# Kernel tuning notes

Measured on AMD Instinct MI355X. Metric: run time of the kernel, lower is better.

Reference implementation:

```python
import jax, jax.numpy as jnp
import numpy as np

EPS = 1e-5
TOP_N = 8
NUM_POINTS = 100
OUT_LO, OUT_HI = 0.0, 1.0


def setup_inputs() -> dict:
    key = jax.random.key(0)
    ks = jax.random.split(key, 7)
    B, D, M, R, MO = 2048, 8, 7, 32768, 9
    x = jax.random.normal(ks[0], (B, D), dtype=jnp.float32)
    # antecedent MF index per (rule, input); -1 means input unused in that rule
    antecedents = jax.random.randint(ks[1], (R, D), 0, M + 1) - 1  # values in [-1, M)
    consequents = jax.random.randint(ks[2], (R,), 0, MO)
    in_centers = jax.random.normal(ks[3], (D, M), dtype=jnp.float32)
    in_widths = 0.2 + 0.3 * jax.random.uniform(ks[4], (D, M), dtype=jnp.float32)
    out_centers = jax.random.uniform(ks[5], (MO,), dtype=jnp.float32)
    out_widths = 0.05 + 0.2 * jax.random.uniform(ks[6], (MO,), dtype=jnp.float32)
    return {"x": x, "antecedents": antecedents, "consequents": consequents,
            "in_centers": in_centers, "in_widths": in_widths,
            "out_centers": out_centers, "out_widths": out_widths}


def reference(x, antecedents, consequents, in_centers, in_widths, out_centers, out_widths):
    B, D = x.shape
    R = antecedents.shape[0]
    M = in_centers.shape[1]

    # Fuzzification: Gaussian input MFs, clamped like the torch module. mu: [B, D, M]
    z = (x[:, :, None] - in_centers[None, :, :]) / in_widths[None, :, :]
    mu = jnp.clip(jnp.exp(-0.5 * z * z), EPS, 1.0)

    # Rule firing strengths: product over inputs of selected memberships ([B, R]).
    # Small fixed loop over D (8) keeps peak memory at one [B, R] temp per step.
    firing = jnp.ones((B, R), dtype=x.dtype)
    for i in range(D):
        idx = antecedents[:, i]                      # [R], -1 => unused
        safe = jnp.clip(idx, 0, M - 1)
        vals = mu[:, i, safe]                        # [B, R]
        firing = firing * jnp.where(idx[None, :] == -1, jnp.ones((), x.dtype), vals)

    top_vals, top_idx = jax.lax.top_k(firing, TOP_N)  # [B, TOP_N]

    # Output universe and output MF table: [MO, P]
    universe = jnp.linspace(OUT_LO, OUT_HI, NUM_POINTS, dtype=x.dtype)
    zo = (universe[None, :] - out_centers[:, None]) / out_widths[:, None]
    out_mu = jnp.exp(-0.5 * zo * zo)

    # Mamdani implication (product) + aggregation (sum) + centroid defuzzification
    cons_top = consequents[top_idx]                   # [B, TOP_N]
    implications = top_vals[:, :, None] * out_mu[cons_top]  # [B, TOP_N, P]
    aggregated = implications.sum(axis=1)             # [B, P]
    numerator = (universe[None, :] * aggregated).sum(axis=1)
    denominator = aggregated.sum(axis=1) + EPS
    return numerator / denominator
```

## Files before the change

### kernel.cpp

```cpp
#include <hip/hip_runtime.h>
#include <math.h>

#define DD 8
#define MM 7
#define MOO 9
#define NPTS 100
#define EPSF 1e-5f

#define THREADS 1024
#define ITERS 8
#define ROWS 8
#define CAP 256
#define WLCAP 8192
#define THR_SLACK 0.9879f

__device__ __forceinline__ float bl(unsigned u) { return __uint_as_float(u << 16); }
__device__ __forceinline__ float bh(unsigned u) { return __uint_as_float(u & 0xFFFF0000u); }
__device__ __forceinline__ unsigned pkb(float a, float b) {
    return (__float_as_uint(b) & 0xFFFF0000u) | (__float_as_uint(a) >> 16);
}

__global__ __launch_bounds__(256) void pack_kernel(const int* __restrict__ ant,
                                                   unsigned* __restrict__ g_off,
                                                   int R) {
    int r = blockIdx.x * 256 + threadIdx.x;
    if (r < R) {
        const int4* a = reinterpret_cast<const int4*>(ant) + (size_t)r * 2;
        int4 lo = a[0], hi = a[1];
        int v[8] = {lo.x, lo.y, lo.z, lo.w, hi.x, hi.y, hi.z, hi.w};
        unsigned code = 0u;
        #pragma unroll
        for (int i = 0; i < 8; ++i) {
            int c = v[i];
            c = (c < 0) ? 7 : (c > MM - 1 ? MM - 1 : c);
            code |= (unsigned)c << (3 * i);
        }
        g_off[r] = ((code & 4095u) << 3) | ((((code >> 12) << 3) + 32768u) << 16);
    }
}

__global__ __launch_bounds__(THREADS, 4) void anfis_scan8(
    const float* __restrict__ x,
    const unsigned* __restrict__ stream_off,
    const float* __restrict__ in_centers,
    const float* __restrict__ in_widths,
    float* __restrict__ g_thr,
    unsigned long long* __restrict__ g_bitmap)
{
    __shared__ uint4 quads[8192];
    __shared__ float mu[ROWS][64];
    __shared__ float pairs[ROWS][256];
    __shared__ uint4 smaxpk[THREADS];
    __shared__ float sT[ROWS];

    const int tid = threadIdx.x;
    const int b0  = blockIdx.x * ROWS;

    if (tid < 512) {
        int row = tid >> 6, d = (tid >> 3) & 7, c = tid & 7;
        float v = 1.0f;
        if (c < MM) {
            float z = (x[(b0 + row) * DD + d] - in_centers[d * MM + c]) / in_widths[d * MM + c];
            v = expf(-0.5f * z * z);
            v = fminf(v, 1.0f);
            v = fmaxf(v, EPSF);
        }
        mu[row][(d << 3) + c] = v;
    }
    __syncthreads();

    #pragma unroll
    for (int i = 0; i < 2; ++i) {
        int k = tid + i * THREADS;
        int row = k >> 8, e = k & 255;
        int p = e >> 6, q = e & 63;
        pairs[row][e] = mu[row][(2 * p) * 8 + (q & 7)] * mu[row][(2 * p + 1) * 8 + (q >> 3)];
    }
    __syncthreads();

    #pragma unroll
    for (int i = 0; i < 8; ++i) {
        int k = tid + i * THREADS;
        int t = k & 4095, h = k >> 12;
        int ia = h * 128 + (t & 63), ib = h * 128 + 64 + ((t >> 6) & 63);
        float q0 = pairs[0][ia] * pairs[0][ib];
        float q1 = pairs[1][ia] * pairs[1][ib];
        float q2 = pairs[2][ia] * pairs[2][ib];
        float q3 = pairs[3][ia] * pairs[3][ib];
        float q4 = pairs[4][ia] * pairs[4][ib];
        float q5 = pairs[5][ia] * pairs[5][ib];
        float q6 = pairs[6][ia] * pairs[6][ib];
        float q7 = pairs[7][ia] * pairs[7][ib];
        quads[k] = make_uint4(pkb(q0, q1), pkb(q2, q3), pkb(q4, q5), pkb(q6, q7));
    }
    __syncthreads();

    const uint4* pk4 = reinterpret_cast<const uint4*>(stream_off);
    float m[ROWS];
    #pragma unroll
    for (int r = 0; r < ROWS; ++r) m[r] = -1.0f;
    #pragma unroll
    for (int j = 0; j < ITERS; ++j) {
        uint4 cd = pk4[j * THREADS + tid];
        unsigned wv_[4] = {cd.x, cd.y, cd.z, cd.w};
        #pragma unroll
        for (int s = 0; s < 4; ++s) {
            unsigned w = wv_[s];
            uint4 eA = quads[(w & 0xFFFFu) >> 3];
            uint4 eB = quads[w >> 19];
            m[0] = fmaxf(m[0], bl(eA.x) * bl(eB.x));
            m[1] = fmaxf(m[1], bh(eA.x) * bh(eB.x));
            m[2] = fmaxf(m[2], bl(eA.y) * bl(eB.y));
            m[3] = fmaxf(m[3], bh(eA.y) * bh(eB.y));
            m[4] = fmaxf(m[4], bl(eA.z) * bl(eB.z));
            m[5] = fmaxf(m[5], bh(eA.z) * bh(eB.z));
            m[6] = fmaxf(m[6], bl(eA.w) * bl(eB.w));
            m[7] = fmaxf(m[7], bh(eA.w) * bh(eB.w));
        }
    }
    smaxpk[tid] = make_uint4(pkb(m[0], m[1]), pkb(m[2], m[3]),
                             pkb(m[4], m[5]), pkb(m[6], m[7]));
    __syncthreads();

    if (tid < 512) {
        int row = tid >> 6, lane = tid & 63;
        float mm[16];
        #pragma unroll
        for (int k = 0; k < 16; ++k) {
            uint4 e = smaxpk[lane + 64 * k];
            unsigned word = (row & 4) ? ((row & 2) ? e.w : e.z)
                                      : ((row & 2) ? e.y : e.x);
            mm[k] = (row & 1) ? bh(word) : bl(word);
        }
        float thr = -1.0f;
        #pragma unroll
        for (int round = 0; round < 8; ++round) {
            float lm = mm[0];
            #pragma unroll
            for (int k = 1; k < 16; ++k) lm = fmaxf(lm, mm[k]);
            float wm = lm;
            #pragma unroll
            for (int off = 32; off >= 1; off >>= 1)
                wm = fmaxf(wm, __shfl_xor(wm, off, 64));
            unsigned long long bal = __ballot(lm == wm);
            int first = (int)__ffsll(bal) - 1;
            if (lane == first) {
                bool done = false;
                #pragma unroll
                for (int k = 0; k < 16; ++k) {
                    bool rm = (!done) && (mm[k] == wm);
                    mm[k] = rm ? -2.0f : mm[k];
                    done = done || rm;
                }
            }
            thr = wm;
        }
        if (lane == 0) sT[row] = thr;
    }
    __syncthreads();

    {
        const int wid = tid >> 6, lane = tid & 63;
        #pragma unroll
        for (int row = 0; row < ROWS; ++row) {
            unsigned long long bal = __ballot(m[row] >= THR_SLACK * sT[row]);
            if (lane == 0)
                g_bitmap[((size_t)blockIdx.x * ROWS + row) * 16 + wid] = bal;
        }
        if (tid < ROWS) g_thr[blockIdx.x * ROWS + tid] = sT[tid];
    }
}

__global__ __launch_bounds__(THREADS, 8) void anfis_select8(
    const float* __restrict__ x,
    const unsigned* __restrict__ stream_off,
    const int* __restrict__ consequents,
    const float* __restrict__ in_centers,
    const float* __restrict__ in_widths,
    const float* __restrict__ out_centers,
    const float* __restrict__ out_widths,
    const float* __restrict__ g_thr,
    const unsigned long long* __restrict__ g_bitmap,
    float* __restrict__ out)
{
    __shared__ float mu[ROWS][64];
    __shared__ float pairs[ROWS][256];
    __shared__ float s0s[MOO], s1s[MOO];
    __shared__ float sT[ROWS];
    __shared__ int   wl[WLCAP];
    __shared__ int   wlcnt;
    __shared__ float cvals[ROWS][CAP];
    __shared__ int   cidx[ROWS][CAP];
    __shared__ int   scnt[ROWS];
    __shared__ float wv[ROWS][8];
    __shared__ int   wc[ROWS][8];

    const int tid = threadIdx.x;
    const int b0  = blockIdx.x * ROWS;

    if (tid < 512) {
        int row = tid >> 6, d = (tid >> 3) & 7, c = tid & 7;
        float v = 1.0f;
        if (c < MM) {
            float z = (x[(b0 + row) * DD + d] - in_centers[d * MM + c]) / in_widths[d * MM + c];
            v = expf(-0.5f * z * z);
            v = fminf(v, 1.0f);
            v = fmaxf(v, EPSF);
        }
        mu[row][(d << 3) + c] = v;
    } else if (tid < 512 + MOO) {
        int mo = tid - 512;
        float oc = out_centers[mo], ow = out_widths[mo];
        float s0 = 0.0f, s1 = 0.0f;
        for (int p = 0; p < NPTS; ++p) {
            float u = (float)p * (1.0f / 99.0f);
            float z = (u - oc) / ow;
            float e = expf(-0.5f * z * z);
            s0 += e;
            s1 += u * e;
        }
        s0s[mo] = s0;
        s1s[mo] = s1;
    } else if (tid >= 544 && tid < 544 + ROWS) {
        sT[tid - 544] = g_thr[blockIdx.x * ROWS + (tid - 544)];
    } else if (tid >= 576 && tid < 576 + ROWS) {
        scnt[tid - 576] = 0;
    } else if (tid == 600) {
        wlcnt = 0;
    }
    __syncthreads();

    #pragma unroll
    for (int i = 0; i < 2; ++i) {
        int k = tid + i * THREADS;
        int row = k >> 8, e = k & 255;
        int p = e >> 6, q = e & 63;
        pairs[row][e] = mu[row][(2 * p) * 8 + (q & 7)] * mu[row][(2 * p + 1) * 8 + (q >> 3)];
    }
    __syncthreads();

    {
        const int wid = tid >> 6, lane = tid & 63;
        #pragma unroll
        for (int row = 0; row < ROWS; ++row) {
            unsigned long long bal = g_bitmap[((size_t)blockIdx.x * ROWS + row) * 16 + wid];
            if ((bal >> lane) & 1ull) {
                int pos = atomicAdd(&wlcnt, 1);
                wl[pos] = (row << 10) | tid;
            }
        }
    }
    __syncthreads();

    {
        const int wid = tid >> 6, lane = tid & 63;
        const int hl = lane & 31;
        const int j = hl >> 2, s = hl & 3;
        const int n = wlcnt;
        for (int i = wid * 2 + (lane >> 5); i < n; i += 32) {
            int it  = wl[i];
            int row = it >> 10;
            int t   = it & 1023;
            int flat = (j * THREADS + t) * 4 + s;
            unsigned w = stream_off[flat];
            unsigned lo12 = (w & 0xFFFFu) >> 3;
            unsigned hi12 = (w >> 19) - 4096u;
            const float* P = pairs[row];
            float f = (P[lo12 & 63u] * P[64 + (lo12 >> 6)])
                    * (P[128 + (hi12 & 63u)] * P[192 + (hi12 >> 6)]);
            if (f >= sT[row]) {
                int pos = atomicAdd(&scnt[row], 1);
                if (pos < CAP) {
                    cvals[row][pos] = f;
                    cidx[row][pos]  = flat;
                }
            }
        }
    }
    __syncthreads();

    if (tid < 512) {
        int row = tid >> 6, lane = tid & 63;
        int n = scnt[row] < CAP ? scnt[row] : CAP;
        for (int c = lane; c < n; c += 64) {
            float v  = cvals[row][c];
            int   id = cidx[row][c];
            int rk = 0;
            for (int mI = 0; mI < n; ++mI) {
                float vm = cvals[row][mI];
                int   im = cidx[row][mI];
                rk += ((vm > v) || (vm == v && im < id)) ? 1 : 0;
            }
            if (rk < 8) {
                wv[row][rk] = v;
                wc[row][rk] = consequents[id];
            }
        }
    }
    __syncthreads();

    if (tid < ROWS) {
        int row = tid;
        float num = 0.0f, den = 0.0f;
        #pragma unroll
        for (int k = 0; k < 8; ++k) {
            num += wv[row][k] * s1s[wc[row][k]];
            den += wv[row][k] * s0s[wc[row][k]];
        }
        out[b0 + row] = num / (den + EPSF);
    }
}

__global__ __launch_bounds__(256) void anfis_kernel(
    const float* __restrict__ x,
    const int* __restrict__ ant,
    const int* __restrict__ consequents,
    const float* __restrict__ in_centers,
    const float* __restrict__ in_widths,
    const float* __restrict__ out_centers,
    const float* __restrict__ out_widths,
    float* __restrict__ out,
    int R)
{
    __shared__ float mu[64];
    __shared__ float pairs[256];
    __shared__ float s0s[MOO], s1s[MOO];
    __shared__ float svals[256][9];
    __shared__ int   sidx[256][9];

    const int tid = threadIdx.x;
    const int b   = blockIdx.x;

    if (tid < 64) {
        int d = tid >> 3, c = tid & 7;
        float v = 1.0f;
        if (c < MM) {
            float z = (x[b * DD + d] - in_centers[d * MM + c]) / in_widths[d * MM + c];
            v = expf(-0.5f * z * z);
            v = fminf(v, 1.0f);
            v = fmaxf(v, EPSF);
        }
        mu[tid] = v;
    } else if (tid < 64 + MOO) {
        int mo = tid - 64;
        float oc = out_centers[mo], ow = out_widths[mo];
        float s0 = 0.0f, s1 = 0.0f;
        for (int p = 0; p < NPTS; ++p) {
            float u = (float)p * (1.0f / 99.0f);
            float z = (u - oc) / ow;
            float e = expf(-0.5f * z * z);
            s0 += e;
            s1 += u * e;
        }
        s0s[mo] = s0;
        s1s[mo] = s1;
    }
    __syncthreads();

    {
        int p = tid >> 6, q = tid & 63;
        pairs[tid] = mu[(2 * p) * 8 + (q & 7)] * mu[(2 * p + 1) * 8 + (q >> 3)];
    }
    __syncthreads();

    float vals[8];
    int   idxs[8];
    #pragma unroll
    for (int k = 0; k < 8; ++k) { vals[k] = -1.0f; idxs[k] = 0x7fffffff; }

    for (int r = tid; r < R; r += 256) {
        const int4* a = reinterpret_cast<const int4*>(ant) + (size_t)r * 2;
        int4 lo = a[0], hi = a[1];
        int v[8] = {lo.x, lo.y, lo.z, lo.w, hi.x, hi.y, hi.z, hi.w};
        unsigned code = 0u;
        #pragma unroll
        for (int i = 0; i < 8; ++i) {
            int c = v[i];
            c = (c < 0) ? 7 : (c > MM - 1 ? MM - 1 : c);
            code |= (unsigned)c << (3 * i);
        }
        float f = pairs[code & 63]
                * pairs[64  + ((code >> 6)  & 63)]
                * pairs[128 + ((code >> 12) & 63)]
                * pairs[192 + ((code >> 18) & 63)];
        if (f > vals[7]) {
            float nv = f; int ni = r;
            #pragma unroll
            for (int k = 0; k < 8; ++k) {
                bool take = nv > vals[k];
                float cv = vals[k]; int ci = idxs[k];
                vals[k] = take ? nv : cv;
                idxs[k] = take ? ni : ci;
                nv = take ? cv : nv;
                ni = take ? ci : ni;
            }
        }
    }

    #pragma unroll
    for (int k = 0; k < 8; ++k) { svals[tid][k] = vals[k]; sidx[tid][k] = idxs[k]; }

    for (int off = 128; off >= 1; off >>= 1) {
        __syncthreads();
        if (tid < off) {
            float ov[8]; int oi[8];
            int pa = 0, pb = 0;
            #pragma unroll
            for (int k = 0; k < 8; ++k) {
                float va = svals[tid][pa];        int ia = sidx[tid][pa];
                float vb = svals[tid + off][pb];  int ib = sidx[tid + off][pb];
                bool ta = (va > vb) || ((va == vb) && (ia < ib));
                ov[k] = ta ? va : vb;
                oi[k] = ta ? ia : ib;
                pa += ta ? 1 : 0;
                pb += ta ? 0 : 1;
            }
            #pragma unroll
            for (int k = 0; k < 8; ++k) { svals[tid][k] = ov[k]; sidx[tid][k] = oi[k]; }
        }
    }
    __syncthreads();

    if (tid == 0) {
        float num = 0.0f, den = 0.0f;
        #pragma unroll
        for (int k = 0; k < 8; ++k) {
            float v = svals[0][k];
            int   c = consequents[sidx[0][k]];
            num += v * s1s[c];
            den += v * s0s[c];
        }
        out[b] = num / (den + EPSF);
    }
}

extern "C" void kernel_launch(void* const* d_in, const int* in_sizes, int n_in,
                              void* d_out, int out_size, void* d_ws, size_t ws_size,
                              hipStream_t stream) {
    const float* x      = (const float*)d_in[0];
    const int*   ant    = (const int*)d_in[1];
    const int*   cons   = (const int*)d_in[2];
    const float* in_c   = (const float*)d_in[3];
    const float* in_w   = (const float*)d_in[4];
    const float* out_c  = (const float*)d_in[5];
    const float* out_w  = (const float*)d_in[6];
    float*       out    = (float*)d_out;

    const int B = in_sizes[0] / DD;
    const int R = in_sizes[1] / DD;

    const int nblk = B / ROWS;
    const bool shape_ok = (R == THREADS * 4 * ITERS) && (B % ROWS == 0);
    const size_t need = (size_t)R * 4 + (size_t)nblk * ROWS * 4
                      + (size_t)nblk * ROWS * 16 * 8;

    if (shape_ok && d_ws && ws_size >= need) {
        unsigned* g_off = (unsigned*)d_ws;
        float*    g_thr = (float*)(g_off + R);
        unsigned long long* g_bitmap = (unsigned long long*)(g_thr + nblk * ROWS);
        pack_kernel<<<(R + 255) / 256, 256, 0, stream>>>(ant, g_off, R);
        anfis_scan8<<<nblk, THREADS, 0, stream>>>(x, g_off, in_c, in_w, g_thr, g_bitmap);
        anfis_select8<<<nblk, THREADS, 0, stream>>>(x, g_off, cons, in_c, in_w,
                                                    out_c, out_w, g_thr, g_bitmap, out);
    } else {
        anfis_kernel<<<B, 256, 0, stream>>>(x, ant, cons, in_c, in_w,
                                            out_c, out_w, out, R);
    }
}
```

Before: 39.52 us.

## Fuse scan and select kernels into one, reusing quads LDS for worklist

Result: faster. 36.16 us (-8.5%).

```diff
diff --git a/kernel.cpp b/kernel.cpp
--- a/kernel.cpp
+++ b/kernel.cpp
@@ -11,7 +11,6 @@
 #define ITERS 8
 #define ROWS 8
 #define CAP 256
-#define WLCAP 8192
 #define THR_SLACK 0.9879f
 
 __device__ __forceinline__ float bl(unsigned u) { return __uint_as_float(u << 16); }
@@ -39,22 +38,33 @@
     }
 }
 
-__global__ __launch_bounds__(THREADS, 4) void anfis_scan8(
+__global__ __launch_bounds__(THREADS, 4) void anfis_fused8(
     const float* __restrict__ x,
     const unsigned* __restrict__ stream_off,
+    const int* __restrict__ consequents,
     const float* __restrict__ in_centers,
     const float* __restrict__ in_widths,
-    float* __restrict__ g_thr,
-    unsigned long long* __restrict__ g_bitmap)
+    const float* __restrict__ out_centers,
+    const float* __restrict__ out_widths,
+    float* __restrict__ out)
 {
     __shared__ uint4 quads[8192];
     __shared__ float mu[ROWS][64];
     __shared__ float pairs[ROWS][256];
     __shared__ uint4 smaxpk[THREADS];
+    __shared__ float s0s[MOO], s1s[MOO];
     __shared__ float sT[ROWS];
+    __shared__ int   scnt[ROWS];
+    __shared__ int   wlcnt;
+    __shared__ float wv[ROWS][8];
+    __shared__ int   wc[ROWS][8];
 
     const int tid = threadIdx.x;
     const int b0  = blockIdx.x * ROWS;
+
+    unsigned short* wl = (unsigned short*)quads;
+    float* cvals = (float*)(quads + 1024);
+    int*   cidx  = (int*)(quads + 1536);
 
     if (tid < 512) {
         int row = tid >> 6, d = (tid >> 3) & 7, c = tid & 7;
@@ -66,6 +76,23 @@
             v = fmaxf(v, EPSF);
         }
         mu[row][(d << 3) + c] = v;
+    } else if (tid < 512 + MOO) {
+        int mo = tid - 512;
+        float oc = out_centers[mo], ow = out_widths[mo];
+        float s0 = 0.0f, s1 = 0.0f;
+        for (int p = 0; p < NPTS; ++p) {
+            float u = (float)p * (1.0f / 99.0f);
+            float z = (u - oc) / ow;
+            float e = expf(-0.5f * z * z);
+            s0 += e;
+            s1 += u * e;
+        }
+        s0s[mo] = s0;
+        s1s[mo] = s1;
+    } else if (tid >= 544 && tid < 544 + ROWS) {
+        scnt[tid - 544] = 0;
+    } else if (tid == 560) {
+        wlcnt = 0;
     }
     __syncthreads();
 
@@ -102,10 +129,10 @@
     #pragma unroll
     for (int j = 0; j < ITERS; ++j) {
         uint4 cd = pk4[j * THREADS + tid];
-        unsigned wv_[4] = {cd.x, cd.y, cd.z, cd.w};
+        unsigned wrd[4] = {cd.x, cd.y, cd.z, cd.w};
         #pragma unroll
         for (int s = 0; s < 4; ++s) {
-            unsigned w = wv_[s];
+            unsigned w = wrd[s];
             uint4 eA = quads[(w & 0xFFFFu) >> 3];
             uint4 eB = quads[w >> 19];
             m[0] = fmaxf(m[0], bl(eA.x) * bl(eB.x));
@@ -160,104 +187,21 @@
     __syncthreads();
 
     {
-        const int wid = tid >> 6, lane = tid & 63;
         #pragma unroll
         for (int row = 0; row < ROWS; ++row) {
-            unsigned long long bal = __ballot(m[row] >= THR_SLACK * sT[row]);
-            if (lane == 0)
-                g_bitmap[((size_t)blockIdx.x * ROWS + row) * 16 + wid] = bal;
-        }
-        if (tid < ROWS) g_thr[blockIdx.x * ROWS + tid] = sT[tid];
-    }
-}
-
-__global__ __launch_bounds__(THREADS, 8) void anfis_select8(
-    const float* __restrict__ x,
-    const unsigned* __restrict__ stream_off,
-    const int* __restrict__ consequents,
-    const float* __restrict__ in_centers,
-    const float* __restrict__ in_widths,
-    const float* __restrict__ out_centers,
-    const float* __restrict__ out_widths,
-    const float* __restrict__ g_thr,
-    const unsigned long long* __restrict__ g_bitmap,
-    float* __restrict__ out)
-{
-    __shared__ float mu[ROWS][64];
-    __shared__ float pairs[ROWS][256];
-    __shared__ float s0s[MOO], s1s[MOO];
-    __shared__ float sT[ROWS];
-    __shared__ int   wl[WLCAP];
-    __shared__ int   wlcnt;
-    __shared__ float cvals[ROWS][CAP];
-    __shared__ int   cidx[ROWS][CAP];
-    __shared__ int   scnt[ROWS];
-    __shared__ float wv[ROWS][8];
-    __shared__ int   wc[ROWS][8];
-
-    const int tid = threadIdx.x;
-    const int b0  = blockIdx.x * ROWS;
-
-    if (tid < 512) {
-        int row = tid >> 6, d = (tid >> 3) & 7, c = tid & 7;
-        float v = 1.0f;
-        if (c < MM) {
-            float z = (x[(b0 + row) * DD + d] - in_centers[d * MM + c]) / in_widths[d * MM + c];
-            v = expf(-0.5f * z * z);
-            v = fminf(v, 1.0f);
-            v = fmaxf(v, EPSF);
-        }
-        mu[row][(d << 3) + c] = v;
-    } else if (tid < 512 + MOO) {
-        int mo = tid - 512;
-        float oc = out_centers[mo], ow = out_widths[mo];
-        float s0 = 0.0f, s1 = 0.0f;
-        for (int p = 0; p < NPTS; ++p) {
-            float u = (float)p * (1.0f / 99.0f);
-            float z = (u - oc) / ow;
-            float e = expf(-0.5f * z * z);
-            s0 += e;
-            s1 += u * e;
-        }
-        s0s[mo] = s0;
-        s1s[mo] = s1;
-    } else if (tid >= 544 && tid < 544 + ROWS) {
-        sT[tid - 544] = g_thr[blockIdx.x * ROWS + (tid - 544)];
-    } else if (tid >= 576 && tid < 576 + ROWS) {
-        scnt[tid - 576] = 0;
-    } else if (tid == 600) {
-        wlcnt = 0;
-    }
-    __syncthreads();
-
-    #pragma unroll
-    for (int i = 0; i < 2; ++i) {
-        int k = tid + i * THREADS;
-        int row = k >> 8, e = k & 255;
-        int p = e >> 6, q = e & 63;
-        pairs[row][e] = mu[row][(2 * p) * 8 + (q & 7)] * mu[row][(2 * p + 1) * 8 + (q >> 3)];
+            if (m[row] >= THR_SLACK * sT[row]) {
+                int pos = atomicAdd(&wlcnt, 1);
+                wl[pos] = (unsigned short)((row << 10) | tid);
+            }
+        }
     }
     __syncthreads();
 
     {
-        const int wid = tid >> 6, lane = tid & 63;
-        #pragma unroll
-        for (int row = 0; row < ROWS; ++row) {
-            unsigned long long bal = g_bitmap[((size_t)blockIdx.x * ROWS + row) * 16 + wid];
-            if ((bal >> lane) & 1ull) {
-                int pos = atomicAdd(&wlcnt, 1);
-                wl[pos] = (row << 10) | tid;
-            }
-        }
-    }
-    __syncthreads();
-
-    {
-        const int wid = tid >> 6, lane = tid & 63;
-        const int hl = lane & 31;
+        const int hl = tid & 31;
         const int j = hl >> 2, s = hl & 3;
         const int n = wlcnt;
-        for (int i = wid * 2 + (lane >> 5); i < n; i += 32) {
+        for (int i = (tid >> 5); i < n; i += 32) {
             int it  = wl[i];
             int row = it >> 10;
             int t   = it & 1023;
@@ -271,8 +215,8 @@
             if (f >= sT[row]) {
                 int pos = atomicAdd(&scnt[row], 1);
                 if (pos < CAP) {
-                    cvals[row][pos] = f;
-                    cidx[row][pos]  = flat;
+                    cvals[row * CAP + pos] = f;
+                    cidx[row * CAP + pos]  = flat;
                 }
             }
         }
@@ -283,12 +227,12 @@
         int row = tid >> 6, lane = tid & 63;
         int n = scnt[row] < CAP ? scnt[row] : CAP;
         for (int c = lane; c < n; c += 64) {
-            float v  = cvals[row][c];
-            int   id = cidx[row][c];
+            float v  = cvals[row * CAP + c];
+            int   id = cidx[row * CAP + c];
             int rk = 0;
             for (int mI = 0; mI < n; ++mI) {
-                float vm = cvals[row][mI];
-                int   im = cidx[row][mI];
+                float vm = cvals[row * CAP + mI];
+                int   im = cidx[row * CAP + mI];
                 rk += ((vm > v) || (vm == v && im < id)) ? 1 : 0;
             }
             if (rk < 8) {
@@ -449,19 +393,14 @@
     const int B = in_sizes[0] / DD;
     const int R = in_sizes[1] / DD;
 
-    const int nblk = B / ROWS;
     const bool shape_ok = (R == THREADS * 4 * ITERS) && (B % ROWS == 0);
-    const size_t need = (size_t)R * 4 + (size_t)nblk * ROWS * 4
-                      + (size_t)nblk * ROWS * 16 * 8;
+    const size_t need = (size_t)R * 4;
 
     if (shape_ok && d_ws && ws_size >= need) {
         unsigned* g_off = (unsigned*)d_ws;
-        float*    g_thr = (float*)(g_off + R);
-        unsigned long long* g_bitmap = (unsigned long long*)(g_thr + nblk * ROWS);
         pack_kernel<<<(R + 255) / 256, 256, 0, stream>>>(ant, g_off, R);
-        anfis_scan8<<<nblk, THREADS, 0, stream>>>(x, g_off, in_c, in_w, g_thr, g_bitmap);
-        anfis_select8<<<nblk, THREADS, 0, stream>>>(x, g_off, cons, in_c, in_w,
-                                                    out_c, out_w, g_thr, g_bitmap, out);
+        anfis_fused8<<<B / ROWS, THREADS, 0, stream>>>(x, g_off, cons, in_c, in_w,
+                                                       out_c, out_w, out);
     } else {
         anfis_kernel<<<B, 256, 0, stream>>>(x, ant, cons, in_c, in_w,
                                             out_c, out_w, out, R);
```
